# Optimization experiments

Measured on AMD Instinct MI355X. Metric: run time of the kernel, lower is better.

## Reference

```python
import jax, jax.numpy as jnp
import numpy as np

EPS = 1e-6      # flow eps buffer
BN_EPS = 1e-5   # torch BatchNorm default eps


def _bn3(x, gamma=None, beta=None):
    # BatchNorm1d on (B, C, N): stats over batch and point dims, training mode
    m = x.mean(axis=(0, 2), keepdims=True)
    v = x.var(axis=(0, 2), keepdims=True)
    xh = (x - m) * jax.lax.rsqrt(v + BN_EPS)
    if gamma is not None:
        xh = xh * gamma[None, :, None] + beta[None, :, None]
    return xh


def _bn2(x, gamma, beta):
    # BatchNorm1d on (B, F): stats over batch dim, training mode
    m = x.mean(axis=0, keepdims=True)
    v = x.var(axis=0, keepdims=True)
    return (x - m) * jax.lax.rsqrt(v + BN_EPS) * gamma[None, :] + beta[None, :]


def _film(g, W0, bn_g, bn_b, W1, b1):
    # Linear(no bias) -> BN -> Swish -> Linear(bias)
    h = g @ W0.T
    h = _bn2(h, bn_g, bn_b)
    h = h * jax.nn.sigmoid(h)  # Swish
    return h @ W1.T + b1


def _warp_branch(p_keep, g, sd0_W, sd0_bn_g, sd0_bn_b, sd1_W,
                 cw_W0, cw_bn_g, cw_bn_b, cw_W1, cw_b1,
                 cb_W0, cb_bn_g, cb_bn_b, cb_W1, cb_b1,
                 sd2_W, sd2_b):
    # T_0: SharedDot -> BN(affine) -> ReLU -> SharedDot -> BN(no affine)
    h = jnp.einsum('oi,bin->bon', sd0_W, p_keep)          # (B, F, N)
    h = jax.nn.relu(_bn3(h, sd0_bn_g, sd0_bn_b))
    h = _bn3(jnp.einsum('oi,bin->bon', sd1_W, h))         # affine=False
    # FiLM conditioning from g
    w = _film(g, cw_W0, cw_bn_g, cw_bn_b, cw_W1, cw_b1)   # (B, F)
    b = _film(g, cb_W0, cb_bn_g, cb_bn_b, cb_W1, cb_b1)   # (B, F)
    h = (EPS + jnp.exp(w))[:, :, None] * h + b[:, :, None]
    # T_1: ReLU -> SharedDot(bias)
    out = jnp.einsum('oi,bin->bon', sd2_W, jax.nn.relu(h)) + sd2_b[None, :, None]
    return out  # (B, n_warp, N)


def setup_inputs() -> dict:
    B, F, G, N = 64, 64, 512, 16384
    key = jax.random.key(0)
    ks = iter(jax.random.split(key, 64))
    d = {
        'p': jax.random.normal(next(ks), (B, 3, N), dtype=jnp.float32),
        'g': jax.random.normal(next(ks), (B, G), dtype=jnp.float32),
    }
    for pre in ('lv', 'mu'):
        d[pre + '_sd0_W'] = 0.1 * jax.random.normal(next(ks), (F, 2), dtype=jnp.float32)
        d[pre + '_sd0_bn_g'] = jnp.ones((F,), jnp.float32)
        d[pre + '_sd0_bn_b'] = jnp.zeros((F,), jnp.float32)
        d[pre + '_sd1_W'] = 0.1 * jax.random.normal(next(ks), (F, F), dtype=jnp.float32)
        for c in ('cw', 'cb'):
            d[pre + '_' + c + '_W0'] = 0.05 * jax.random.normal(next(ks), (F, G), dtype=jnp.float32)
            d[pre + '_' + c + '_bn_g'] = jnp.ones((F,), jnp.float32)
            d[pre + '_' + c + '_bn_b'] = jnp.zeros((F,), jnp.float32)
            d[pre + '_' + c + '_W1'] = 0.01 * jax.random.normal(next(ks), (F, F), dtype=jnp.float32)
            d[pre + '_' + c + '_b1'] = jnp.zeros((F,), jnp.float32)
        d[pre + '_sd2_W'] = 0.01 * jax.random.normal(next(ks), (1, F), dtype=jnp.float32)
        d[pre + '_sd2_b'] = jnp.zeros((1,), jnp.float32)
    return d


def reference(p, g,
              lv_sd0_W, lv_sd0_bn_g, lv_sd0_bn_b, lv_sd1_W,
              lv_cw_W0, lv_cw_bn_g, lv_cw_bn_b, lv_cw_W1, lv_cw_b1,
              lv_cb_W0, lv_cb_bn_g, lv_cb_bn_b, lv_cb_W1, lv_cb_b1,
              lv_sd2_W, lv_sd2_b,
              mu_sd0_W, mu_sd0_bn_g, mu_sd0_bn_b, mu_sd1_W,
              mu_cw_W0, mu_cw_bn_g, mu_cw_bn_b, mu_cw_W1, mu_cw_b1,
              mu_cb_W0, mu_cb_bn_g, mu_cb_bn_b, mu_cb_W1, mu_cb_b1,
              mu_sd2_W, mu_sd2_b):
    # warp_inds=[0], keep_inds=[1,2]
    p_keep = p[:, 1:3, :]
    lv_w = jax.nn.soft_sign(_warp_branch(
        p_keep, g, lv_sd0_W, lv_sd0_bn_g, lv_sd0_bn_b, lv_sd1_W,
        lv_cw_W0, lv_cw_bn_g, lv_cw_bn_b, lv_cw_W1, lv_cw_b1,
        lv_cb_W0, lv_cb_bn_g, lv_cb_bn_b, lv_cb_W1, lv_cb_b1,
        lv_sd2_W, lv_sd2_b))
    mu_w = _warp_branch(
        p_keep, g, mu_sd0_W, mu_sd0_bn_g, mu_sd0_bn_b, mu_sd1_W,
        mu_cw_W0, mu_cw_bn_g, mu_cw_bn_b, mu_cw_W1, mu_cw_b1,
        mu_cb_W0, mu_cb_bn_g, mu_cb_bn_b, mu_cb_W1, mu_cb_b1,
        mu_sd2_W, mu_sd2_b)
    logvar = jnp.zeros_like(p).at[:, 0:1, :].set(lv_w)
    mu = jnp.zeros_like(p).at[:, 0:1, :].set(mu_w)
    # mode='direct'
    p_out = jnp.sqrt(EPS + jnp.exp(logvar)) * p + mu
    return p_out, mu, logvar
```

## Files before the change

kernel.cpp:

```cpp
#include <hip/hip_runtime.h>
#include <math.h>

#define BB 64
#define FF 64
#define GG 512
#define NN 16384
#define PTOT (BB*NN)
#define EPSF 1e-6f
#define BN_EPSF 1e-5f

#define WS_HBUF   0
#define WS_MOM    16384
#define WS_H2S1   16392
#define WS_H2S2   16520
#define WS_COEF   16648
#define WS_M2     17160
#define WS_RS2    17288
#define WS_FILMW  17416
#define WS_FILMB  25608
#define WS_WB     33800
#define WS_PC     37896
#define WS_PART   70664
#define WS_ZERO_FLOATS 16648

#define OFF_MU  (BB*3*NN)
#define OFF_LV  (2*BB*3*NN)

typedef __attribute__((ext_vector_type(8))) short short8_t;
typedef __attribute__((ext_vector_type(4))) float f32x4;

__device__ __forceinline__ unsigned int bf16u(float x) {
    unsigned int u = __float_as_uint(x);
    return ((u + 0x7FFFu + ((u >> 16) & 1u)) >> 16) & 0xFFFFu;
}

__global__ __launch_bounds__(256) void k_filmA(
    const float* __restrict__ g,
    const float* __restrict__ W0_0, const float* __restrict__ W0_1,
    const float* __restrict__ W0_2, const float* __restrict__ W0_3,
    float* __restrict__ ws) {
    __shared__ float g_tile[64][65];
    __shared__ float wT[64][69];
    const int combo = blockIdx.x;
    const int kbase = blockIdx.y * 64;
    const int t = threadIdx.x;
    const float* W0 = combo==0 ? W0_0 : combo==1 ? W0_1 : combo==2 ? W0_2 : W0_3;
    float* hb = ws + WS_HBUF + combo*4096;

#pragma unroll
    for (int n = 0; n < 4; ++n) {
        const int idx = t + n*256;
        const int row = idx >> 4, k4 = idx & 15;
        const float4 gv = *(const float4*)(g  + row*GG + kbase + k4*4);
        const float4 wv = *(const float4*)(W0 + row*GG + kbase + k4*4);
        g_tile[row][k4*4+0] = gv.x; g_tile[row][k4*4+1] = gv.y;
        g_tile[row][k4*4+2] = gv.z; g_tile[row][k4*4+3] = gv.w;
        wT[k4*4+0][row] = wv.x; wT[k4*4+1][row] = wv.y;
        wT[k4*4+2][row] = wv.z; wT[k4*4+3][row] = wv.w;
    }
    __syncthreads();

    const int b0 = (t >> 3) * 2, f0 = (t & 7) * 8;
    float acc[2][8];
#pragma unroll
    for (int i = 0; i < 2; ++i)
#pragma unroll
        for (int j = 0; j < 8; ++j) acc[i][j] = 0.f;
#pragma unroll 4
    for (int k = 0; k < 64; ++k) {
        const float g0 = g_tile[b0][k], g1 = g_tile[b0+1][k];
        const float4 w01 = *(const float4*)&wT[k][f0];
        const float4 w23 = *(const float4*)&wT[k][f0+4];
        const float wv[8] = {w01.x,w01.y,w01.z,w01.w,w23.x,w23.y,w23.z,w23.w};
#pragma unroll
        for (int j = 0; j < 8; ++j) {
            acc[0][j] = fmaf(g0, wv[j], acc[0][j]);
            acc[1][j] = fmaf(g1, wv[j], acc[1][j]);
        }
    }
#pragma unroll
    for (int i = 0; i < 2; ++i)
#pragma unroll
        for (int j = 0; j < 8; ++j)
            atomicAdd(&hb[(b0+i)*64 + f0+j], acc[i][j]);
}

__global__ __launch_bounds__(256) void k_filmB(
    const float* __restrict__ bng_0, const float* __restrict__ bnb_0,
    const float* __restrict__ W1_0,  const float* __restrict__ b1_0,
    const float* __restrict__ bng_1, const float* __restrict__ bnb_1,
    const float* __restrict__ W1_1,  const float* __restrict__ b1_1,
    const float* __restrict__ bng_2, const float* __restrict__ bnb_2,
    const float* __restrict__ W1_2,  const float* __restrict__ b1_2,
    const float* __restrict__ bng_3, const float* __restrict__ bnb_3,
    const float* __restrict__ W1_3,  const float* __restrict__ b1_3,
    float* __restrict__ ws) {
    __shared__ float H[64][65];
    __shared__ float S[64][65];
    __shared__ float W1T[64][69];
    const int combo = blockIdx.x;
    const int t = threadIdx.x;
    const float* bng = combo==0 ? bng_0 : combo==1 ? bng_1 : combo==2 ? bng_2 : bng_3;
    const float* bnb = combo==0 ? bnb_0 : combo==1 ? bnb_1 : combo==2 ? bnb_2 : bnb_3;
    const float* W1  = combo==0 ? W1_0  : combo==1 ? W1_1  : combo==2 ? W1_2  : W1_3;
    const float* b1  = combo==0 ? b1_0  : combo==1 ? b1_1  : combo==2 ? b1_2  : b1_3;
    const float* hb  = ws + WS_HBUF + combo*4096;
    float* outp = ws + ((combo & 1) ? WS_FILMB : WS_FILMW) + (combo >> 1) * 4096;

    for (int idx = t; idx < 4096; idx += 256) H[idx >> 6][idx & 63] = hb[idx];
    {
#pragma unroll
        for (int n = 0; n < 4; ++n) {
            const int idx = t + n*256;
            const int f2 = idx >> 4, k4 = idx & 15;
            const float4 wv = *(const float4*)(W1 + f2*64 + k4*4);
            W1T[k4*4+0][f2] = wv.x; W1T[k4*4+1][f2] = wv.y;
            W1T[k4*4+2][f2] = wv.z; W1T[k4*4+3][f2] = wv.w;
        }
    }
    __syncthreads();
    for (int idx = t; idx < 4096; idx += 256) {
        const int b = idx >> 6, f = idx & 63;
        float m = 0.f;
        for (int b2 = 0; b2 < 64; ++b2) m += H[b2][f];
        m *= (1.f/64.f);
        float v = 0.f;
        for (int b2 = 0; b2 < 64; ++b2) { const float d = H[b2][f] - m; v = fmaf(d, d, v); }
        v *= (1.f/64.f);
        const float xh = (H[b][f] - m) * rsqrtf(v + BN_EPSF) * bng[f] + bnb[f];
        S[b][f] = xh / (1.f + expf(-xh));
    }
    __syncthreads();
    const int b0 = (t >> 3) * 2, f0 = (t & 7) * 8;
    float acc[2][8];
#pragma unroll
    for (int i = 0; i < 2; ++i)
#pragma unroll
        for (int j = 0; j < 8; ++j) acc[i][j] = 0.f;
#pragma unroll 4
    for (int k = 0; k < 64; ++k) {
        const float s0 = S[b0][k], s1 = S[b0+1][k];
        const float4 w01 = *(const float4*)&W1T[k][f0];
        const float4 w23 = *(const float4*)&W1T[k][f0+4];
        const float wv[8] = {w01.x,w01.y,w01.z,w01.w,w23.x,w23.y,w23.z,w23.w};
#pragma unroll
        for (int j = 0; j < 8; ++j) {
            acc[0][j] = fmaf(s0, wv[j], acc[0][j]);
            acc[1][j] = fmaf(s1, wv[j], acc[1][j]);
        }
    }
#pragma unroll
    for (int i = 0; i < 2; ++i)
#pragma unroll
        for (int j = 0; j < 8; ++j)
            outp[(b0+i)*64 + f0+j] = acc[i][j] + b1[f0+j];
}

__global__ __launch_bounds__(256) void k_moments(const float* __restrict__ p, float* __restrict__ ws) {
    __shared__ float red[4][8];
    const int t = threadIdx.x;
    const int gid = blockIdx.x * 256 + t;
    const int pos8 = gid << 3;
    const int b = pos8 >> 14, n = pos8 & 16383;
    const float* base = p + (size_t)b*3*NN + NN + n;
    const float4 ua = *(const float4*)base;
    const float4 ub = *(const float4*)(base + 4);
    const float4 va = *(const float4*)(base + NN);
    const float4 vb = *(const float4*)(base + NN + 4);
    float su  = (ua.x+ua.y)+(ua.z+ua.w)+(ub.x+ub.y)+(ub.z+ub.w);
    float sv  = (va.x+va.y)+(va.z+va.w)+(vb.x+vb.y)+(vb.z+vb.w);
    float suu = fmaf(ua.x,ua.x, fmaf(ua.y,ua.y, fmaf(ua.z,ua.z, ua.w*ua.w)))
              + fmaf(ub.x,ub.x, fmaf(ub.y,ub.y, fmaf(ub.z,ub.z, ub.w*ub.w)));
    float svv = fmaf(va.x,va.x, fmaf(va.y,va.y, fmaf(va.z,va.z, va.w*va.w)))
              + fmaf(vb.x,vb.x, fmaf(vb.y,vb.y, fmaf(vb.z,vb.z, vb.w*vb.w)));
    float suv = fmaf(ua.x,va.x, fmaf(ua.y,va.y, fmaf(ua.z,va.z, ua.w*va.w)))
              + fmaf(ub.x,vb.x, fmaf(ub.y,vb.y, fmaf(ub.z,vb.z, ub.w*vb.w)));
#pragma unroll
    for (int off = 32; off > 0; off >>= 1) {
        su  += __shfl_down(su,  off);
        sv  += __shfl_down(sv,  off);
        suu += __shfl_down(suu, off);
        svv += __shfl_down(svv, off);
        suv += __shfl_down(suv, off);
    }
    const int w = t >> 6;
    if ((t & 63) == 0) {
        red[w][0] = su; red[w][1] = sv; red[w][2] = suu; red[w][3] = svv; red[w][4] = suv;
    }
    __syncthreads();
    if (t < 5)
        atomicAdd(&ws[WS_MOM + t], red[0][t] + red[1][t] + red[2][t] + red[3][t]);
}

__global__ __launch_bounds__(256) void k_coef2(const float* __restrict__ lvW, const float* __restrict__ lvG,
                                               const float* __restrict__ lvB, const float* __restrict__ muW,
                                               const float* __restrict__ muG, const float* __restrict__ muB,
                                               const float* __restrict__ lvW1, const float* __restrict__ muW1,
                                               float* __restrict__ ws) {
    const int t = threadIdx.x;
    const int bid = blockIdx.x;
    if (bid == 0 && t < 128) {
        const int br = t >> 6, c = t & 63;
        const float* W  = br ? muW : lvW;
        const float* Gp = br ? muG : lvG;
        const float* Bp = br ? muB : lvB;
        const float inv = 1.f / (float)PTOT;
        const float Eu  = ws[WS_MOM+0]*inv, Ev  = ws[WS_MOM+1]*inv;
        const float Euu = ws[WS_MOM+2]*inv, Evv = ws[WS_MOM+3]*inv, Euv = ws[WS_MOM+4]*inv;
        const float w0 = W[c*2 + 0], w1 = W[c*2 + 1];
        const float m   = w0*Eu + w1*Ev;
        const float e2  = w0*w0*Euu + 2.f*w0*w1*Euv + w1*w1*Evv;
        const float var = e2 - m*m;
        const float rs  = rsqrtf(var + BN_EPSF);
        const float ga = Gp[c], be = Bp[c];
        float4 cf;
        cf.x = w0*rs*ga; cf.y = w1*rs*ga; cf.z = be - m*rs*ga; cf.w = 0.f;
        *(float4*)(ws + WS_COEF + (br*64+c)*4) = cf;
    }
    unsigned short* wb = (unsigned short*)(ws + WS_WB);
    for (int e = bid*2048 + t; e < bid*2048 + 2048; e += 256) {
        const int brx = e >> 12, r = e & 4095;
        wb[e] = (unsigned short)bf16u((brx ? muW1 : lvW1)[r]);
    }
}

__global__ __launch_bounds__(256) void k_h2stats(const float* __restrict__ p, float* __restrict__ ws) {
    __shared__ float uS[1024], vS[1024];
    __shared__ float red1[2][4][64];
    __shared__ float red2[2][4][64];
    const int t = threadIdx.x;
    const int bid = blockIdx.x;
    const int b = bid >> 4;
    const int n0 = (bid & 15) * 1024;
    const float* pk = p + (size_t)b*3*NN + NN;
    *(float4*)&uS[t*4] = *(const float4*)(pk + n0 + t*4);
    *(float4*)&vS[t*4] = *(const float4*)(pk + NN + n0 + t*4);
    __syncthreads();
    const int w = t >> 6, lane = t & 63, g = lane >> 4, col = lane & 15;
    const unsigned short* wbg = (const unsigned short*)(ws + WS_WB);

#pragma unroll 1
    for (int br = 0; br < 2; ++br) {
        float cA[16], cB[16], cC[16];
#pragma unroll
        for (int kt = 0; kt < 2; ++kt)
#pragma unroll
            for (int j = 0; j < 8; ++j) {
                const int i = kt*8 + j, ch = kt*32 + g*8 + j;
                const float4 cf = *(const float4*)(ws + WS_COEF + (br*64 + ch)*4);
                cA[i] = cf.x; cB[i] = cf.y; cC[i] = cf.z;
            }
        short8_t a[4][2];
#pragma unroll
        for (int mt = 0; mt < 4; ++mt)
#pragma unroll
            for (int kt = 0; kt < 2; ++kt)
                a[mt][kt] = *(const short8_t*)(wbg + br*4096 + (mt*16+col)*64 + kt*32 + g*8);
        float s1v[16], s2v[16];
#pragma unroll
        for (int i = 0; i < 16; ++i) { s1v[i] = 0.f; s2v[i] = 0.f; }

#pragma unroll 4
        for (int nt = 0; nt < 16; ++nt) {
            const int pl = (nt*4 + w)*16 + col;
            const float u = uS[pl], v = vS[pl];
            union { uint4 u4; short8_t s8; } bf[2];
#pragma unroll
            for (int kt = 0; kt < 2; ++kt) {
                unsigned int dw[4];
#pragma unroll
                for (int q = 0; q < 4; ++q) {
                    const int i0 = kt*8 + q*2;
                    const float h0 = fmaxf(fmaf(cA[i0],   u, fmaf(cB[i0],   v, cC[i0])),   0.f);
                    const float h1 = fmaxf(fmaf(cA[i0+1], u, fmaf(cB[i0+1], v, cC[i0+1])), 0.f);
                    asm("v_cvt_pk_bf16_f32 %0, %1, %2" : "=v"(dw[q]) : "v"(h0), "v"(h1));
                }
                bf[kt].u4 = make_uint4(dw[0], dw[1], dw[2], dw[3]);
            }
            f32x4 acc[4];
#pragma unroll
            for (int mt = 0; mt < 4; ++mt) { f32x4 z = {0.f,0.f,0.f,0.f}; acc[mt] = z; }
#pragma unroll
            for (int mt = 0; mt < 4; ++mt) {
                acc[mt] = __builtin_amdgcn_mfma_f32_16x16x32_bf16(a[mt][0], bf[0].s8, acc[mt], 0,0,0);
                acc[mt] = __builtin_amdgcn_mfma_f32_16x16x32_bf16(a[mt][1], bf[1].s8, acc[mt], 0,0,0);
            }
#pragma unroll
            for (int mt = 0; mt < 4; ++mt)
#pragma unroll
                for (int r = 0; r < 4; ++r) {
                    const int i = mt*4 + r;
                    const float x = acc[mt][r];
                    s1v[i] += x;
                    s2v[i] = fmaf(x, x, s2v[i]);
                }
        }
#pragma unroll
        for (int i = 0; i < 16; ++i) {
#pragma unroll
            for (int off = 1; off <= 8; off <<= 1) {
                s1v[i] += __shfl_xor(s1v[i], off);
                s2v[i] += __shfl_xor(s2v[i], off);
            }
        }
        if (col == 0) {
#pragma unroll
            for (int mt = 0; mt < 4; ++mt)
#pragma unroll
                for (int r = 0; r < 4; ++r) {
                    const int c = mt*16 + g*4 + r;
                    red1[br][w][c] = s1v[mt*4+r];
                    red2[br][w][c] = s2v[mt*4+r];
                }
        }
    }
    __syncthreads();
    {
        const int kind = t >> 6, c = t & 63;
        const int br2 = kind >> 1, sk = kind & 1;
        const float* rr = sk ? &red2[br2][0][0] : &red1[br2][0][0];
        ws[WS_PART + bid*256 + (br2*2 + sk)*64 + c] =
            rr[0*64 + c] + rr[1*64 + c] + rr[2*64 + c] + rr[3*64 + c];
    }
}

__global__ __launch_bounds__(256) void k_red(float* __restrict__ ws) {
    __shared__ float a1[4], a2[4];
    const int idx = blockIdx.x;
    const int br = idx >> 6, c = idx & 63;
    const int t = threadIdx.x;
    float s1 = 0.f, s2 = 0.f;
    for (int j = t; j < 1024; j += 256) {
        const float* pp = ws + WS_PART + j*256;
        s1 += pp[(br*2 + 0)*64 + c];
        s2 += pp[(br*2 + 1)*64 + c];
    }
#pragma unroll
    for (int off = 32; off > 0; off >>= 1) {
        s1 += __shfl_down(s1, off);
        s2 += __shfl_down(s2, off);
    }
    if ((t & 63) == 0) { a1[t >> 6] = s1; a2[t >> 6] = s2; }
    __syncthreads();
    if (t == 0) {
        const float S1 = a1[0]+a1[1]+a1[2]+a1[3];
        const float S2 = a2[0]+a2[1]+a2[2]+a2[3];
        const float inv = 1.f / (float)PTOT;
        const float m2 = S1 * inv, e2 = S2 * inv;
        ws[WS_M2  + idx] = m2;
        ws[WS_RS2 + idx] = rsqrtf(e2 - m2*m2 + BN_EPSF);
    }
}

__global__ __launch_bounds__(256) void k_finstats(const float* __restrict__ lv_sd2W,
                                                  const float* __restrict__ mu_sd2W,
                                                  float* __restrict__ ws) {
    __shared__ float m2S[128], rsS[128];
    const int t = threadIdx.x;
    const int bid = blockIdx.x;
    if (t < 128) { m2S[t] = ws[WS_M2 + t]; rsS[t] = ws[WS_RS2 + t]; }
    __syncthreads();
    for (int e = bid*512 + t; e < bid*512 + 512; e += 256) {
        const int br = e >> 12, rem = e & 4095, c = rem & 63;
        const float fw  = ws[WS_FILMW + br*4096 + rem];
        const float fb  = ws[WS_FILMB + br*4096 + rem];
        const float rs2 = rsS[br*64 + c];
        const float m2  = m2S[br*64 + c];
        const float s = (EPSF + expf(fw)) * rs2;
        float4 pc;
        pc.x = s; pc.y = fb - s*m2; pc.z = (br ? mu_sd2W : lv_sd2W)[c]; pc.w = 0.f;
        *(float4*)(ws + WS_PC + e*4) = pc;
    }
}

__global__ __launch_bounds__(256) void k_main(
    const float* __restrict__ p,
    const float* __restrict__ lv_sd2b, const float* __restrict__ mu_sd2b,
    const float* __restrict__ ws, float* __restrict__ out)
{
    __shared__ float xS[1024], uS[1024], vS[1024];
    __shared__ __align__(16) float pcS[2][64][4];
    __shared__ float resS[1024];

    const int t   = threadIdx.x;
    const int bid = blockIdx.x;
    const int b   = bid >> 4;
    const int n0  = (bid & 15) * 1024;
    const size_t pb = (size_t)b * 3 * NN;
    const float* pk = p + pb + NN;

    *(float4*)&xS[t*4] = *(const float4*)(p + pb + n0 + t*4);
    *(float4*)&uS[t*4] = *(const float4*)(pk + n0 + t*4);
    *(float4*)&vS[t*4] = *(const float4*)(pk + NN + n0 + t*4);
    if (t < 128) {
        const int br = t >> 6, c = t & 63;
        *(float4*)&pcS[br][c][0] = *(const float4*)(ws + WS_PC + ((br*64 + b)*64 + c)*4);
    }
    __syncthreads();

    const int w = t >> 6, lane = t & 63, g = lane >> 4, col = lane & 15;
    const unsigned short* wbg = (const unsigned short*)(ws + WS_WB);
    const float sd2b0 = lv_sd2b[0], sd2b1 = mu_sd2b[0];

#pragma unroll 1
    for (int br = 0; br < 2; ++br) {
        float cA[16], cB[16], cC[16];
#pragma unroll
        for (int kt = 0; kt < 2; ++kt)
#pragma unroll
            for (int j = 0; j < 8; ++j) {
                const int i = kt*8 + j, ch = kt*32 + g*8 + j;
                const float4 cf = *(const float4*)(ws + WS_COEF + (br*64 + ch)*4);
                cA[i] = cf.x; cB[i] = cf.y; cC[i] = cf.z;
            }
        short8_t a[4][2];
#pragma unroll
        for (int mt = 0; mt < 4; ++mt)
#pragma unroll
            for (int kt = 0; kt < 2; ++kt)
                a[mt][kt] = *(const short8_t*)(wbg + br*4096 + (mt*16+col)*64 + kt*32 + g*8);
        float sp[16], tq[16], w2v[16];
#pragma unroll
        for (int mt = 0; mt < 4; ++mt)
#pragma unroll
            for (int r = 0; r < 4; ++r) {
                const int i = mt*4 + r, c = mt*16 + g*4 + r;
                const float4 pc = *(const float4*)&pcS[br][c][0];
                sp[i] = pc.x; tq[i] = pc.y; w2v[i] = pc.z;
            }

#pragma unroll 4
        for (int nt = 0; nt < 16; ++nt) {
            const int pl = (nt*4 + w)*16 + col;
            const float u = uS[pl], v = vS[pl];
            union { uint4 u4; short8_t s8; } bf[2];
#pragma unroll
            for (int kt = 0; kt < 2; ++kt) {
                unsigned int dw[4];
#pragma unroll
                for (int q = 0; q < 4; ++q) {
                    const int i0 = kt*8 + q*2;
                    const float h0 = fmaxf(fmaf(cA[i0],   u, fmaf(cB[i0],   v, cC[i0])),   0.f);
                    const float h1 = fmaxf(fmaf(cA[i0+1], u, fmaf(cB[i0+1], v, cC[i0+1])), 0.f);
                    asm("v_cvt_pk_bf16_f32 %0, %1, %2" : "=v"(dw[q]) : "v"(h0), "v"(h1));
                }
                bf[kt].u4 = make_uint4(dw[0], dw[1], dw[2], dw[3]);
            }
            f32x4 acc[4];
#pragma unroll
            for (int mt = 0; mt < 4; ++mt) { f32x4 z = {0.f,0.f,0.f,0.f}; acc[mt] = z; }
#pragma unroll
            for (int mt = 0; mt < 4; ++mt) {
                acc[mt] = __builtin_amdgcn_mfma_f32_16x16x32_bf16(a[mt][0], bf[0].s8, acc[mt], 0,0,0);
                acc[mt] = __builtin_amdgcn_mfma_f32_16x16x32_bf16(a[mt][1], bf[1].s8, acc[mt], 0,0,0);
            }
            float po0 = 0.f, po1 = 0.f;
#pragma unroll
            for (int mt = 0; mt < 4; ++mt)
#pragma unroll
                for (int r = 0; r < 4; r += 2) {
                    const int i = mt*4 + r;
                    const float hf0 = fmaf(acc[mt][r],   sp[i],   tq[i]);
                    const float hf1 = fmaf(acc[mt][r+1], sp[i+1], tq[i+1]);
                    po0 = fmaf(fmaxf(hf0, 0.f), w2v[i],   po0);
                    po1 = fmaf(fmaxf(hf1, 0.f), w2v[i+1], po1);
                }
            float po = po0 + po1;
            po += __shfl_xor(po, 16);
            po += __shfl_xor(po, 32);
            if (br == 0) {
                if (lane < 16) resS[pl] = po;
            } else {
                const float ol = resS[pl] + sd2b0;
                const float om = po + sd2b1;
                const float lw = ol / (1.f + fabsf(ol));
                const float sc = sqrtf(EPSF + expf(lw));
                const size_t nix = pb + n0 + pl;
                if (g == 0) {
                    out[nix] = fmaf(sc, xS[pl], om);
                } else if (g == 1) {
                    out[OFF_MU + nix] = om;
                } else if (g == 2) {
                    out[OFF_LV + nix] = lw;
                }
            }
        }
    }
    const float S1 = sqrtf(1.f + EPSF);
#pragma unroll
    for (int e = 0; e < 4; ++e) {
        const int j = e*256 + t;
        const size_t ix1 = pb + (size_t)NN + n0 + j;
        const size_t ix2 = pb + (size_t)2*NN + n0 + j;
        out[ix1]          = S1 * uS[j];
        out[OFF_MU + ix1] = 0.f;
        out[OFF_LV + ix1] = 0.f;
        out[ix2]          = S1 * vS[j];
        out[OFF_MU + ix2] = 0.f;
        out[OFF_LV + ix2] = 0.f;
    }
}

extern "C" void kernel_launch(void* const* d_in, const int* in_sizes, int n_in,
                              void* d_out, int out_size, void* d_ws, size_t ws_size,
                              hipStream_t stream) {
    (void)in_sizes; (void)n_in; (void)out_size; (void)ws_size;
    const float* p = (const float*)d_in[0];
    const float* g = (const float*)d_in[1];
#define IN(i) ((const float*)d_in[i])
    float* ws  = (float*)d_ws;
    float* out = (float*)d_out;

    hipMemsetAsync(d_ws, 0, WS_ZERO_FLOATS * sizeof(float), stream);

    hipLaunchKernelGGL(k_filmA, dim3(4, 8), dim3(256), 0, stream,
                       g, IN(6), IN(11), IN(22), IN(27), ws);
    hipLaunchKernelGGL(k_filmB, dim3(4),    dim3(256), 0, stream,
                       IN(7),  IN(8),  IN(9),  IN(10),
                       IN(12), IN(13), IN(14), IN(15),
                       IN(23), IN(24), IN(25), IN(26),
                       IN(28), IN(29), IN(30), IN(31),
                       ws);
    hipLaunchKernelGGL(k_moments, dim3(512),  dim3(256), 0, stream, p, ws);
    hipLaunchKernelGGL(k_coef2,   dim3(4),    dim3(256), 0, stream,
                       IN(2), IN(3), IN(4), IN(18), IN(19), IN(20), IN(5), IN(21), ws);
    hipLaunchKernelGGL(k_h2stats, dim3(1024), dim3(256), 0, stream, p, ws);
    hipLaunchKernelGGL(k_red,     dim3(128),  dim3(256), 0, stream, ws);
    hipLaunchKernelGGL(k_finstats, dim3(16),  dim3(256), 0, stream, IN(16), IN(32), ws);
    hipLaunchKernelGGL(k_main,    dim3(1024), dim3(256), 0, stream,
                       p, IN(17), IN(33), ws, out);
#undef IN
}
```

Baseline: 140.3 us.

## Use packed FP32 math in hot loops, interleave u/v in LDS, fuse reduction kernels

The elementwise FMA, ReLU-input and statistics accumulation in k_h2stats and k_main now use v_pk_fma_f32/v_pk_add_f32 on channel pairs, which halves the VALU instruction count in the per-point loops. u and v are interleaved in shared memory so one 8-byte LDS read fetches both. The k_red and k_finstats kernels are merged into a single k_redpc kernel, removing one launch and the workspace round trip. The packing and unpacking of vector pairs may add register moves that eat into the savings.

```diff
diff --git a/kernel.cpp b/kernel.cpp
--- a/kernel.cpp
+++ b/kernel.cpp
@@ -11,11 +11,7 @@
 
 #define WS_HBUF   0
 #define WS_MOM    16384
-#define WS_H2S1   16392
-#define WS_H2S2   16520
 #define WS_COEF   16648
-#define WS_M2     17160
-#define WS_RS2    17288
 #define WS_FILMW  17416
 #define WS_FILMB  25608
 #define WS_WB     33800
@@ -28,10 +24,21 @@
 
 typedef __attribute__((ext_vector_type(8))) short short8_t;
 typedef __attribute__((ext_vector_type(4))) float f32x4;
+typedef __attribute__((ext_vector_type(2))) float f32x2;
 
 __device__ __forceinline__ unsigned int bf16u(float x) {
     unsigned int u = __float_as_uint(x);
     return ((u + 0x7FFFu + ((u >> 16) & 1u)) >> 16) & 0xFFFFu;
+}
+__device__ __forceinline__ f32x2 pk_fma(f32x2 a, f32x2 b, f32x2 c) {
+    f32x2 d;
+    asm("v_pk_fma_f32 %0, %1, %2, %3" : "=v"(d) : "v"(a), "v"(b), "v"(c));
+    return d;
+}
+__device__ __forceinline__ f32x2 pk_add(f32x2 a, f32x2 b) {
+    f32x2 d;
+    asm("v_pk_add_f32 %0, %1, %2" : "=v"(d) : "v"(a), "v"(b));
+    return d;
 }
 
 __global__ __launch_bounds__(256) void k_filmA(
@@ -225,7 +232,7 @@
 }
 
 __global__ __launch_bounds__(256) void k_h2stats(const float* __restrict__ p, float* __restrict__ ws) {
-    __shared__ float uS[1024], vS[1024];
+    __shared__ __align__(16) float uvS[1024][2];
     __shared__ float red1[2][4][64];
     __shared__ float red2[2][4][64];
     const int t = threadIdx.x;
@@ -233,22 +240,31 @@
     const int b = bid >> 4;
     const int n0 = (bid & 15) * 1024;
     const float* pk = p + (size_t)b*3*NN + NN;
-    *(float4*)&uS[t*4] = *(const float4*)(pk + n0 + t*4);
-    *(float4*)&vS[t*4] = *(const float4*)(pk + NN + n0 + t*4);
+    {
+        const float4 u4 = *(const float4*)(pk + n0 + t*4);
+        const float4 v4 = *(const float4*)(pk + NN + n0 + t*4);
+        float4 a0; a0.x = u4.x; a0.y = v4.x; a0.z = u4.y; a0.w = v4.y;
+        float4 a1; a1.x = u4.z; a1.y = v4.z; a1.z = u4.w; a1.w = v4.w;
+        *(float4*)&uvS[t*4][0]     = a0;
+        *(float4*)&uvS[t*4 + 2][0] = a1;
+    }
     __syncthreads();
     const int w = t >> 6, lane = t & 63, g = lane >> 4, col = lane & 15;
     const unsigned short* wbg = (const unsigned short*)(ws + WS_WB);
 
 #pragma unroll 1
     for (int br = 0; br < 2; ++br) {
-        float cA[16], cB[16], cC[16];
+        f32x2 cA2[8], cB2[8], cC2[8];
 #pragma unroll
         for (int kt = 0; kt < 2; ++kt)
 #pragma unroll
-            for (int j = 0; j < 8; ++j) {
-                const int i = kt*8 + j, ch = kt*32 + g*8 + j;
-                const float4 cf = *(const float4*)(ws + WS_COEF + (br*64 + ch)*4);
-                cA[i] = cf.x; cB[i] = cf.y; cC[i] = cf.z;
+            for (int q = 0; q < 4; ++q) {
+                const int pi = kt*4 + q, ch = kt*32 + g*8 + q*2;
+                const float4 c0 = *(const float4*)(ws + WS_COEF + (br*64 + ch)*4);
+                const float4 c1 = *(const float4*)(ws + WS_COEF + (br*64 + ch + 1)*4);
+                cA2[pi] = (f32x2){c0.x, c1.x};
+                cB2[pi] = (f32x2){c0.y, c1.y};
+                cC2[pi] = (f32x2){c0.z, c1.z};
             }
         short8_t a[4][2];
 #pragma unroll
@@ -256,23 +272,26 @@
 #pragma unroll
             for (int kt = 0; kt < 2; ++kt)
                 a[mt][kt] = *(const short8_t*)(wbg + br*4096 + (mt*16+col)*64 + kt*32 + g*8);
-        float s1v[16], s2v[16];
-#pragma unroll
-        for (int i = 0; i < 16; ++i) { s1v[i] = 0.f; s2v[i] = 0.f; }
+        f32x2 s1v[8], s2v[8];
+#pragma unroll
+        for (int i = 0; i < 8; ++i) { s1v[i] = (f32x2){0.f,0.f}; s2v[i] = (f32x2){0.f,0.f}; }
 
 #pragma unroll 4
         for (int nt = 0; nt < 16; ++nt) {
             const int pl = (nt*4 + w)*16 + col;
-            const float u = uS[pl], v = vS[pl];
+            const f32x2 uv = *(const f32x2*)&uvS[pl][0];
+            const f32x2 uu = (f32x2){uv.x, uv.x};
+            const f32x2 vv = (f32x2){uv.y, uv.y};
             union { uint4 u4; short8_t s8; } bf[2];
 #pragma unroll
             for (int kt = 0; kt < 2; ++kt) {
                 unsigned int dw[4];
 #pragma unroll
                 for (int q = 0; q < 4; ++q) {
-                    const int i0 = kt*8 + q*2;
-                    const float h0 = fmaxf(fmaf(cA[i0],   u, fmaf(cB[i0],   v, cC[i0])),   0.f);
-                    const float h1 = fmaxf(fmaf(cA[i0+1], u, fmaf(cB[i0+1], v, cC[i0+1])), 0.f);
+                    const int pi = kt*4 + q;
+                    const f32x2 h2v = pk_fma(cA2[pi], uu, pk_fma(cB2[pi], vv, cC2[pi]));
+                    const float h0 = fmaxf(h2v.x, 0.f);
+                    const float h1 = fmaxf(h2v.y, 0.f);
                     asm("v_cvt_pk_bf16_f32 %0, %1, %2" : "=v"(dw[q]) : "v"(h0), "v"(h1));
                 }
                 bf[kt].u4 = make_uint4(dw[0], dw[1], dw[2], dw[3]);
@@ -288,20 +307,25 @@
 #pragma unroll
             for (int mt = 0; mt < 4; ++mt)
 #pragma unroll
-                for (int r = 0; r < 4; ++r) {
-                    const int i = mt*4 + r;
-                    const float x = acc[mt][r];
-                    s1v[i] += x;
-                    s2v[i] = fmaf(x, x, s2v[i]);
+                for (int rr = 0; rr < 2; ++rr) {
+                    const int pi = mt*2 + rr;
+                    const f32x2 xp = (f32x2){acc[mt][rr*2], acc[mt][rr*2+1]};
+                    s1v[pi] = pk_add(s1v[pi], xp);
+                    s2v[pi] = pk_fma(xp, xp, s2v[pi]);
                 }
         }
 #pragma unroll
-        for (int i = 0; i < 16; ++i) {
+        for (int pi = 0; pi < 8; ++pi) {
+            float a1x = s1v[pi].x, a1y = s1v[pi].y, a2x = s2v[pi].x, a2y = s2v[pi].y;
 #pragma unroll
             for (int off = 1; off <= 8; off <<= 1) {
-                s1v[i] += __shfl_xor(s1v[i], off);
-                s2v[i] += __shfl_xor(s2v[i], off);
-            }
+                a1x += __shfl_xor(a1x, off);
+                a1y += __shfl_xor(a1y, off);
+                a2x += __shfl_xor(a2x, off);
+                a2y += __shfl_xor(a2y, off);
+            }
+            s1v[pi] = (f32x2){a1x, a1y};
+            s2v[pi] = (f32x2){a2x, a2y};
         }
         if (col == 0) {
 #pragma unroll
@@ -309,8 +333,9 @@
 #pragma unroll
                 for (int r = 0; r < 4; ++r) {
                     const int c = mt*16 + g*4 + r;
-                    red1[br][w][c] = s1v[mt*4+r];
-                    red2[br][w][c] = s2v[mt*4+r];
+                    const int pi = mt*2 + (r >> 1);
+                    red1[br][w][c] = (r & 1) ? s1v[pi].y : s1v[pi].x;
+                    red2[br][w][c] = (r & 1) ? s2v[pi].y : s2v[pi].x;
                 }
         }
     }
@@ -324,8 +349,11 @@
     }
 }
 
-__global__ __launch_bounds__(256) void k_red(float* __restrict__ ws) {
+__global__ __launch_bounds__(256) void k_redpc(const float* __restrict__ lv_sd2W,
+                                               const float* __restrict__ mu_sd2W,
+                                               float* __restrict__ ws) {
     __shared__ float a1[4], a2[4];
+    __shared__ float stats[2];
     const int idx = blockIdx.x;
     const int br = idx >> 6, c = idx & 63;
     const int t = threadIdx.x;
@@ -347,29 +375,19 @@
         const float S2 = a2[0]+a2[1]+a2[2]+a2[3];
         const float inv = 1.f / (float)PTOT;
         const float m2 = S1 * inv, e2 = S2 * inv;
-        ws[WS_M2  + idx] = m2;
-        ws[WS_RS2 + idx] = rsqrtf(e2 - m2*m2 + BN_EPSF);
-    }
-}
-
-__global__ __launch_bounds__(256) void k_finstats(const float* __restrict__ lv_sd2W,
-                                                  const float* __restrict__ mu_sd2W,
-                                                  float* __restrict__ ws) {
-    __shared__ float m2S[128], rsS[128];
-    const int t = threadIdx.x;
-    const int bid = blockIdx.x;
-    if (t < 128) { m2S[t] = ws[WS_M2 + t]; rsS[t] = ws[WS_RS2 + t]; }
-    __syncthreads();
-    for (int e = bid*512 + t; e < bid*512 + 512; e += 256) {
-        const int br = e >> 12, rem = e & 4095, c = rem & 63;
-        const float fw  = ws[WS_FILMW + br*4096 + rem];
-        const float fb  = ws[WS_FILMB + br*4096 + rem];
-        const float rs2 = rsS[br*64 + c];
-        const float m2  = m2S[br*64 + c];
+        stats[0] = m2;
+        stats[1] = rsqrtf(e2 - m2*m2 + BN_EPSF);
+    }
+    __syncthreads();
+    if (t < 64) {
+        const int b = t;
+        const float m2  = stats[0], rs2 = stats[1];
+        const float fw  = ws[WS_FILMW + br*4096 + b*64 + c];
+        const float fb  = ws[WS_FILMB + br*4096 + b*64 + c];
         const float s = (EPSF + expf(fw)) * rs2;
         float4 pc;
         pc.x = s; pc.y = fb - s*m2; pc.z = (br ? mu_sd2W : lv_sd2W)[c]; pc.w = 0.f;
-        *(float4*)(ws + WS_PC + e*4) = pc;
+        *(float4*)(ws + WS_PC + ((br*64 + b)*64 + c)*4) = pc;
     }
 }
 
@@ -378,7 +396,8 @@
     const float* __restrict__ lv_sd2b, const float* __restrict__ mu_sd2b,
     const float* __restrict__ ws, float* __restrict__ out)
 {
-    __shared__ float xS[1024], uS[1024], vS[1024];
+    __shared__ float xS[1024];
+    __shared__ __align__(16) float uvS[1024][2];
     __shared__ __align__(16) float pcS[2][64][4];
     __shared__ float resS[1024];
 
@@ -390,8 +409,14 @@
     const float* pk = p + pb + NN;
 
     *(float4*)&xS[t*4] = *(const float4*)(p + pb + n0 + t*4);
-    *(float4*)&uS[t*4] = *(const float4*)(pk + n0 + t*4);
-    *(float4*)&vS[t*4] = *(const float4*)(pk + NN + n0 + t*4);
+    {
+        const float4 u4 = *(const float4*)(pk + n0 + t*4);
+        const float4 v4 = *(const float4*)(pk + NN + n0 + t*4);
+        float4 a0; a0.x = u4.x; a0.y = v4.x; a0.z = u4.y; a0.w = v4.y;
+        float4 a1; a1.x = u4.z; a1.y = v4.z; a1.z = u4.w; a1.w = v4.w;
+        *(float4*)&uvS[t*4][0]     = a0;
+        *(float4*)&uvS[t*4 + 2][0] = a1;
+    }
     if (t < 128) {
         const int br = t >> 6, c = t & 63;
         *(float4*)&pcS[br][c][0] = *(const float4*)(ws + WS_PC + ((br*64 + b)*64 + c)*4);
@@ -404,14 +429,17 @@
 
 #pragma unroll 1
     for (int br = 0; br < 2; ++br) {
-        float cA[16], cB[16], cC[16];
+        f32x2 cA2[8], cB2[8], cC2[8];
 #pragma unroll
         for (int kt = 0; kt < 2; ++kt)
 #pragma unroll
-            for (int j = 0; j < 8; ++j) {
-                const int i = kt*8 + j, ch = kt*32 + g*8 + j;
-                const float4 cf = *(const float4*)(ws + WS_COEF + (br*64 + ch)*4);
-                cA[i] = cf.x; cB[i] = cf.y; cC[i] = cf.z;
+            for (int q = 0; q < 4; ++q) {
+                const int pi = kt*4 + q, ch = kt*32 + g*8 + q*2;
+                const float4 c0 = *(const float4*)(ws + WS_COEF + (br*64 + ch)*4);
+                const float4 c1 = *(const float4*)(ws + WS_COEF + (br*64 + ch + 1)*4);
+                cA2[pi] = (f32x2){c0.x, c1.x};
+                cB2[pi] = (f32x2){c0.y, c1.y};
+                cC2[pi] = (f32x2){c0.z, c1.z};
             }
         short8_t a[4][2];
 #pragma unroll
@@ -419,29 +447,35 @@
 #pragma unroll
             for (int kt = 0; kt < 2; ++kt)
                 a[mt][kt] = *(const short8_t*)(wbg + br*4096 + (mt*16+col)*64 + kt*32 + g*8);
-        float sp[16], tq[16], w2v[16];
+        f32x2 sp2[8], tq2[8], w2v2[8];
 #pragma unroll
         for (int mt = 0; mt < 4; ++mt)
 #pragma unroll
-            for (int r = 0; r < 4; ++r) {
-                const int i = mt*4 + r, c = mt*16 + g*4 + r;
-                const float4 pc = *(const float4*)&pcS[br][c][0];
-                sp[i] = pc.x; tq[i] = pc.y; w2v[i] = pc.z;
+            for (int rr = 0; rr < 2; ++rr) {
+                const int pi = mt*2 + rr, c0i = mt*16 + g*4 + rr*2;
+                const float4 p0 = *(const float4*)&pcS[br][c0i][0];
+                const float4 p1 = *(const float4*)&pcS[br][c0i+1][0];
+                sp2[pi]  = (f32x2){p0.x, p1.x};
+                tq2[pi]  = (f32x2){p0.y, p1.y};
+                w2v2[pi] = (f32x2){p0.z, p1.z};
             }
 
 #pragma unroll 4
         for (int nt = 0; nt < 16; ++nt) {
             const int pl = (nt*4 + w)*16 + col;
-            const float u = uS[pl], v = vS[pl];
+            const f32x2 uv = *(const f32x2*)&uvS[pl][0];
+            const f32x2 uu = (f32x2){uv.x, uv.x};
+            const f32x2 vv = (f32x2){uv.y, uv.y};
             union { uint4 u4; short8_t s8; } bf[2];
 #pragma unroll
             for (int kt = 0; kt < 2; ++kt) {
                 unsigned int dw[4];
 #pragma unroll
                 for (int q = 0; q < 4; ++q) {
-                    const int i0 = kt*8 + q*2;
-                    const float h0 = fmaxf(fmaf(cA[i0],   u, fmaf(cB[i0],   v, cC[i0])),   0.f);
-                    const float h1 = fmaxf(fmaf(cA[i0+1], u, fmaf(cB[i0+1], v, cC[i0+1])), 0.f);
+                    const int pi = kt*4 + q;
+                    const f32x2 h2v = pk_fma(cA2[pi], uu, pk_fma(cB2[pi], vv, cC2[pi]));
+                    const float h0 = fmaxf(h2v.x, 0.f);
+                    const float h1 = fmaxf(h2v.y, 0.f);
                     asm("v_cvt_pk_bf16_f32 %0, %1, %2" : "=v"(dw[q]) : "v"(h0), "v"(h1));
                 }
                 bf[kt].u4 = make_uint4(dw[0], dw[1], dw[2], dw[3]);
@@ -454,18 +488,18 @@
                 acc[mt] = __builtin_amdgcn_mfma_f32_16x16x32_bf16(a[mt][0], bf[0].s8, acc[mt], 0,0,0);
                 acc[mt] = __builtin_amdgcn_mfma_f32_16x16x32_bf16(a[mt][1], bf[1].s8, acc[mt], 0,0,0);
             }
-            float po0 = 0.f, po1 = 0.f;
+            f32x2 po2 = (f32x2){0.f, 0.f};
 #pragma unroll
             for (int mt = 0; mt < 4; ++mt)
 #pragma unroll
-                for (int r = 0; r < 4; r += 2) {
-                    const int i = mt*4 + r;
-                    const float hf0 = fmaf(acc[mt][r],   sp[i],   tq[i]);
-                    const float hf1 = fmaf(acc[mt][r+1], sp[i+1], tq[i+1]);
-                    po0 = fmaf(fmaxf(hf0, 0.f), w2v[i],   po0);
-                    po1 = fmaf(fmaxf(hf1, 0.f), w2v[i+1], po1);
+                for (int rr = 0; rr < 2; ++rr) {
+                    const int pi = mt*2 + rr;
+                    f32x2 hf = pk_fma((f32x2){acc[mt][rr*2], acc[mt][rr*2+1]}, sp2[pi], tq2[pi]);
+                    hf.x = fmaxf(hf.x, 0.f);
+                    hf.y = fmaxf(hf.y, 0.f);
+                    po2 = pk_fma(hf, w2v2[pi], po2);
                 }
-            float po = po0 + po1;
+            float po = po2.x + po2.y;
             po += __shfl_xor(po, 16);
             po += __shfl_xor(po, 32);
             if (br == 0) {
@@ -492,10 +526,10 @@
         const int j = e*256 + t;
         const size_t ix1 = pb + (size_t)NN + n0 + j;
         const size_t ix2 = pb + (size_t)2*NN + n0 + j;
-        out[ix1]          = S1 * uS[j];
+        out[ix1]          = S1 * uvS[j][0];
         out[OFF_MU + ix1] = 0.f;
         out[OFF_LV + ix1] = 0.f;
-        out[ix2]          = S1 * vS[j];
+        out[ix2]          = S1 * uvS[j][1];
         out[OFF_MU + ix2] = 0.f;
         out[OFF_LV + ix2] = 0.f;
     }
@@ -525,8 +559,7 @@
     hipLaunchKernelGGL(k_coef2,   dim3(4),    dim3(256), 0, stream,
                        IN(2), IN(3), IN(4), IN(18), IN(19), IN(20), IN(5), IN(21), ws);
     hipLaunchKernelGGL(k_h2stats, dim3(1024), dim3(256), 0, stream, p, ws);
-    hipLaunchKernelGGL(k_red,     dim3(128),  dim3(256), 0, stream, ws);
-    hipLaunchKernelGGL(k_finstats, dim3(16),  dim3(256), 0, stream, IN(16), IN(32), ws);
+    hipLaunchKernelGGL(k_redpc,   dim3(128),  dim3(256), 0, stream, IN(16), IN(32), ws);
     hipLaunchKernelGGL(k_main,    dim3(1024), dim3(256), 0, stream,
                        p, IN(17), IN(33), ws, out);
 #undef IN
```

Result: slower. 146.4 us (+4.4%).
